# Kernel optimization log

Hardware: AMD Instinct MI355X
Metric: run time of the kernel (lower is better)

## Reference

```python
import jax, jax.numpy as jnp
import numpy as np

K = 2
LAMBDA_ALPHA = 1.0
LAMBDA_BETA = 0.5


def setup_inputs() -> dict:
    key = jax.random.key(0)
    k1, k2, k3, k4, k5 = jax.random.split(key, 5)
    bs, C, H, W = 32, 256, 64, 64
    R = 8
    hid = C // R  # 32
    x = jax.random.normal(k1, (bs, C, H, W), dtype=jnp.float32)
    # fc1: Linear(C -> C/R)
    w1 = jax.random.normal(k2, (hid, C), dtype=jnp.float32) * 0.05
    b1 = jnp.zeros((hid,), dtype=jnp.float32)
    # fc2: k Linears(hid -> 2C), stacked on leading k axis
    w2 = jax.random.normal(k3, (K, 2 * C, hid), dtype=jnp.float32) * 0.05
    b2 = jax.random.normal(k4, (K, 2 * C), dtype=jnp.float32) * 0.05
    return {"x": x, "w1": w1, "b1": b1, "w2": w2, "b2": b2}


def reference(x, w1, b1, w2, b2):
    # Residual branch: global avg pool -> fc1 -> relu -> k fc2 heads -> 2*sigmoid-1
    pooled = x.mean(axis=(2, 3))                       # [bs, C]
    h = jax.nn.relu(pooled @ w1.T + b1)                # [bs, hid]
    delta = 2.0 * jax.nn.sigmoid(
        jnp.einsum('koh,bh->bko', w2, h) + b2[None]) - 1.0  # [bs, k, 2C]
    alpha = delta[..., 0::2]                           # [bs, k, C] (even cols)
    beta = delta[..., 1::2]                            # [bs, k, C] (odd cols)
    init_alpha = jnp.array([1.0, 0.0], dtype=x.dtype)  # init_alpha[0]=1
    init_beta = jnp.array([1.0, 0.0], dtype=x.dtype)   # init_beta[0]=1 (as in source)
    a = init_alpha[None, :, None] + LAMBDA_ALPHA * alpha  # [bs, k, C]
    b = init_beta[None, :, None] + LAMBDA_BETA * beta     # [bs, k, C]
    # broadcasted per-(b,c) affine, max over k branches
    y = x[:, None] * a[..., None, None] + b[..., None, None]  # [bs, k, C, H, W]
    return jnp.max(y, axis=1)                                  # [bs, C, H, W]
```

## Files before the change

kernel.cpp:

```cpp
#include <hip/hip_runtime.h>


#define BS   32
#define CCH  256
#define HW   4096
#define HID  32
#define KK   2

__global__ __launch_bounds__(256) void pool_kernel(const float* __restrict__ x,
                                                   float* __restrict__ pooled) {
    const int bc = blockIdx.x;
    const float4* xp = (const float4*)(x + (size_t)bc * HW);
    const int t = threadIdx.x;
    float s = 0.f;
#pragma unroll
    for (int i = 0; i < 4; ++i) {
        float4 v = xp[t + i * 256];
        s += (v.x + v.y) + (v.z + v.w);
    }
#pragma unroll
    for (int off = 32; off > 0; off >>= 1)
        s += __shfl_down(s, off, 64);
    __shared__ float ws[4];
    if ((t & 63) == 0) ws[t >> 6] = s;
    __syncthreads();
    if (t == 0) {
        float tot = (ws[0] + ws[1]) + (ws[2] + ws[3]);
        pooled[bc] = tot * (1.0f / HW);
    }
}

__global__ __launch_bounds__(256) void coef_kernel(const float* __restrict__ pooled,
                                                   const float* __restrict__ w1,
                                                   const float* __restrict__ b1,
                                                   const float* __restrict__ w2,
                                                   const float* __restrict__ b2,
                                                   float* __restrict__ A,
                                                   float* __restrict__ Bc) {
    const int b = blockIdx.x;
    const int t = threadIdx.x;
    __shared__ float pl[CCH];
    __shared__ float h[HID];
    if (t < CCH) pl[t] = pooled[b * CCH + t];
    __syncthreads();
    if (t < HID) {
        float s = b1[t];
        const float* w1r = w1 + t * CCH;
        for (int c = 0; c < CCH; ++c) s += pl[c] * w1r[c];
        h[t] = s > 0.f ? s : 0.f;
    }
    __syncthreads();
    for (int idx = t; idx < KK * 2 * CCH; idx += 256) {
        const int k = idx >> 9;
        const int o = idx & 511;
        float s = b2[k * 2 * CCH + o];
        const float* w2p = w2 + (size_t)(k * 2 * CCH + o) * HID;
#pragma unroll
        for (int j = 0; j < HID; ++j) s += w2p[j] * h[j];
        const float d = 2.f / (1.f + expf(-s)) - 1.f;
        const int c = o >> 1;
        const float initv = (k == 0) ? 1.f : 0.f;
        if ((o & 1) == 0)
            A[(b * KK + k) * CCH + c] = initv + 1.0f * d;
        else
            Bc[(b * KK + k) * CCH + c] = initv + 0.5f * d;
    }
}

__global__ __launch_bounds__(256) void apply_kernel(const float* __restrict__ x,
                                                    const float* __restrict__ A,
                                                    const float* __restrict__ Bc,
                                                    float* __restrict__ out) {
    const size_t i4 = (size_t)blockIdx.x * 256 + threadIdx.x;
    const int bc = (int)(i4 >> 10);
    const int b = bc >> 8;
    const int c = bc & 255;
    const float a0 = A[(b * 2 + 0) * CCH + c];
    const float a1 = A[(b * 2 + 1) * CCH + c];
    const float b0 = Bc[(b * 2 + 0) * CCH + c];
    const float b1 = Bc[(b * 2 + 1) * CCH + c];
    const float4 v = ((const float4*)x)[i4];
    float4 r;
    r.x = fmaxf(v.x * a0 + b0, v.x * a1 + b1);
    r.y = fmaxf(v.y * a0 + b0, v.y * a1 + b1);
    r.z = fmaxf(v.z * a0 + b0, v.z * a1 + b1);
    r.w = fmaxf(v.w * a0 + b0, v.w * a1 + b1);
    ((float4*)out)[i4] = r;
}

extern "C" void kernel_launch(void* const* d_in, const int* in_sizes, int n_in,
                              void* d_out, int out_size, void* d_ws, size_t ws_size,
                              hipStream_t stream) {
    const float* x  = (const float*)d_in[0];
    const float* w1 = (const float*)d_in[1];
    const float* b1 = (const float*)d_in[2];
    const float* w2 = (const float*)d_in[3];
    const float* b2 = (const float*)d_in[4];
    float* out = (float*)d_out;

    float* pooled = (float*)d_ws;
    float* A      = pooled + BS * CCH;
    float* Bc     = A + BS * KK * CCH;

    pool_kernel<<<BS * CCH, 256, 0, stream>>>(x, pooled);
    coef_kernel<<<BS, 256, 0, stream>>>(pooled, w1, b1, w2, b2, A, Bc);
    const int n4 = (BS * CCH * HW) / 4;
    apply_kernel<<<n4 / 256, 256, 0, stream>>>(x, A, Bc, out);
}
```

Baseline: 260.3 us.

## Fuse pooling and coefficient MLP via last-block atomic counter; nontemporal output stores

The pooling and coefficient kernels are merged into one launch. Each block increments a per-batch atomic counter, and the last block for a batch computes that batch's MLP, with the fc1 dot products split across all 256 threads. The apply kernel now writes its output with nontemporal stores, and the sigmoid uses the fast __expf. This drops one kernel launch and the serial 32-thread fc1 loop, in exchange for an added memset, atomics and fences.

```diff
diff --git a/kernel.cpp b/kernel.cpp
--- a/kernel.cpp
+++ b/kernel.cpp
@@ -5,13 +5,26 @@
 #define CCH  256
 #define HW   4096
 #define HID  32
-#define KK   2
 
-__global__ __launch_bounds__(256) void pool_kernel(const float* __restrict__ x,
-                                                   float* __restrict__ pooled) {
-    const int bc = blockIdx.x;
+typedef float vfloat4 __attribute__((ext_vector_type(4)));
+
+__global__ __launch_bounds__(256) void pool_coef_kernel(
+    const float* __restrict__ x,
+    const float* __restrict__ w1,
+    const float* __restrict__ b1,
+    const float* __restrict__ w2,
+    const float* __restrict__ b2,
+    int*   __restrict__ cnt,
+    float* __restrict__ pooled,
+    float* __restrict__ A,
+    float* __restrict__ Bc)
+{
+    const int bc   = blockIdx.x;
+    const int b    = bc >> 8;
+    const int t    = threadIdx.x;
+    const int lane = t & 63, wave = t >> 6;
+
     const float4* xp = (const float4*)(x + (size_t)bc * HW);
-    const int t = threadIdx.x;
     float s = 0.f;
 #pragma unroll
     for (int i = 0; i < 4; ++i) {
@@ -21,49 +34,55 @@
 #pragma unroll
     for (int off = 32; off > 0; off >>= 1)
         s += __shfl_down(s, off, 64);
-    __shared__ float ws[4];
-    if ((t & 63) == 0) ws[t >> 6] = s;
+
+    __shared__ float wsum[4];
+    __shared__ int   isLast;
+    if (lane == 0) wsum[wave] = s;
     __syncthreads();
     if (t == 0) {
-        float tot = (ws[0] + ws[1]) + (ws[2] + ws[3]);
-        pooled[bc] = tot * (1.0f / HW);
+        pooled[bc] = (wsum[0] + wsum[1] + wsum[2] + wsum[3]) * (1.f / HW);
+        __threadfence();
+        int old = atomicAdd(&cnt[b], 1);
+        isLast = (old == CCH - 1);
     }
-}
+    __syncthreads();
+    if (!isLast) return;
 
-__global__ __launch_bounds__(256) void coef_kernel(const float* __restrict__ pooled,
-                                                   const float* __restrict__ w1,
-                                                   const float* __restrict__ b1,
-                                                   const float* __restrict__ w2,
-                                                   const float* __restrict__ b2,
-                                                   float* __restrict__ A,
-                                                   float* __restrict__ Bc) {
-    const int b = blockIdx.x;
-    const int t = threadIdx.x;
+    __threadfence();
     __shared__ float pl[CCH];
-    __shared__ float h[HID];
-    if (t < CCH) pl[t] = pooled[b * CCH + t];
+    __shared__ float hpart[256];
+    __shared__ float hval[HID];
+    pl[t] = ((volatile const float*)pooled)[b * CCH + t];
+    __syncthreads();
+    {
+        const int hid = t >> 3, part = t & 7;
+        float s2 = 0.f;
+        const float* w1p = w1 + hid * CCH + part * 32;
+        const float* plp = pl + part * 32;
+#pragma unroll
+        for (int j = 0; j < 32; ++j) s2 += plp[j] * w1p[j];
+        hpart[t] = s2;
+    }
     __syncthreads();
     if (t < HID) {
-        float s = b1[t];
-        const float* w1r = w1 + t * CCH;
-        for (int c = 0; c < CCH; ++c) s += pl[c] * w1r[c];
-        h[t] = s > 0.f ? s : 0.f;
+        float s2 = b1[t];
+#pragma unroll
+        for (int p = 0; p < 8; ++p) s2 += hpart[t * 8 + p];
+        hval[t] = s2 > 0.f ? s2 : 0.f;
     }
     __syncthreads();
-    for (int idx = t; idx < KK * 2 * CCH; idx += 256) {
+    for (int idx = t; idx < 2 * 2 * CCH; idx += 256) {
         const int k = idx >> 9;
         const int o = idx & 511;
-        float s = b2[k * 2 * CCH + o];
-        const float* w2p = w2 + (size_t)(k * 2 * CCH + o) * HID;
+        float s2 = b2[k * 512 + o];
+        const float* w2p = w2 + (size_t)(k * 512 + o) * HID;
 #pragma unroll
-        for (int j = 0; j < HID; ++j) s += w2p[j] * h[j];
-        const float d = 2.f / (1.f + expf(-s)) - 1.f;
+        for (int j = 0; j < HID; ++j) s2 += w2p[j] * hval[j];
+        const float d = 2.f / (1.f + __expf(-s2)) - 1.f;
         const int c = o >> 1;
         const float initv = (k == 0) ? 1.f : 0.f;
-        if ((o & 1) == 0)
-            A[(b * KK + k) * CCH + c] = initv + 1.0f * d;
-        else
-            Bc[(b * KK + k) * CCH + c] = initv + 0.5f * d;
+        if ((o & 1) == 0) A [(b * 2 + k) * CCH + c] = initv + d;
+        else              Bc[(b * 2 + k) * CCH + c] = initv + 0.5f * d;
     }
 }
 
@@ -75,17 +94,17 @@
     const int bc = (int)(i4 >> 10);
     const int b = bc >> 8;
     const int c = bc & 255;
-    const float a0 = A[(b * 2 + 0) * CCH + c];
-    const float a1 = A[(b * 2 + 1) * CCH + c];
+    const float a0 = A [(b * 2 + 0) * CCH + c];
+    const float a1 = A [(b * 2 + 1) * CCH + c];
     const float b0 = Bc[(b * 2 + 0) * CCH + c];
     const float b1 = Bc[(b * 2 + 1) * CCH + c];
     const float4 v = ((const float4*)x)[i4];
-    float4 r;
+    vfloat4 r;
     r.x = fmaxf(v.x * a0 + b0, v.x * a1 + b1);
     r.y = fmaxf(v.y * a0 + b0, v.y * a1 + b1);
     r.z = fmaxf(v.z * a0 + b0, v.z * a1 + b1);
     r.w = fmaxf(v.w * a0 + b0, v.w * a1 + b1);
-    ((float4*)out)[i4] = r;
+    __builtin_nontemporal_store(r, (vfloat4*)out + i4);
 }
 
 extern "C" void kernel_launch(void* const* d_in, const int* in_sizes, int n_in,
@@ -98,12 +117,14 @@
     const float* b2 = (const float*)d_in[4];
     float* out = (float*)d_out;
 
-    float* pooled = (float*)d_ws;
+    int*   cnt    = (int*)d_ws;
+    float* pooled = (float*)d_ws + 32;
     float* A      = pooled + BS * CCH;
-    float* Bc     = A + BS * KK * CCH;
+    float* Bc     = A + BS * 2 * CCH;
 
-    pool_kernel<<<BS * CCH, 256, 0, stream>>>(x, pooled);
-    coef_kernel<<<BS, 256, 0, stream>>>(pooled, w1, b1, w2, b2, A, Bc);
+    (void)hipMemsetAsync(cnt, 0, BS * sizeof(int), stream);
+    pool_coef_kernel<<<BS * CCH, 256, 0, stream>>>(x, w1, b1, w2, b2,
+                                                   cnt, pooled, A, Bc);
     const int n4 = (BS * CCH * HW) / 4;
     apply_kernel<<<n4 / 256, 256, 0, stream>>>(x, A, Bc, out);
 }
```

Result: slower. 651.5 us (+150.3%).
